# Optimization experiments

Measured on AMD Instinct MI355X. Metric: run time of the kernel, lower is better.

Reference implementation:

```python
import jax, jax.numpy as jnp
import numpy as np

B, Hc, Wc, C, NH, SR, WS = 4, 64, 64, 256, 8, 2, 4
N = Hc * Wc


def _window_partition(x, ws, H, W):
    # x: (B, h, N, d) -> (B*h*nWin, ws*ws, d)
    Bb, h, _, d = x.shape
    x = x.reshape(Bb * h, H // ws, ws, W // ws, ws, d)
    x = x.transpose(0, 1, 3, 2, 4, 5)
    return x.reshape(-1, ws * ws, d)


def _window_reverse(win, ws, H, W, head):
    nwin = (H // ws) * (W // ws)
    Bh = win.shape[0] // nwin
    x = win.reshape(Bh, H // ws, W // ws, ws, ws, -1).transpose(0, 1, 3, 2, 4, 5).reshape(Bh, H, W, -1)
    Bb = Bh // head
    x = x.reshape(Bb, head, H, W, -1).transpose(0, 2, 3, 1, 4)  # heads interleave into channels
    return x.reshape(Bb, H * W, -1)


def _layernorm(x, w, b):
    m = x.mean(-1, keepdims=True)
    v = x.var(-1, keepdims=True)
    return (x - m) / jnp.sqrt(v + 1e-5) * w + b


def setup_inputs() -> dict:
    key = jax.random.key(0)
    ks = jax.random.split(key, 16)
    lin = lambda k, i, o: 0.02 * jax.random.normal(k, (i, o), jnp.float32)
    inp = {
        'x': jax.random.normal(ks[0], (B, N, C), jnp.float32),
        'q1_w': lin(ks[1], C, C // 2), 'q1_b': jnp.zeros((C // 2,), jnp.float32),
        'kv1_w': lin(ks[2], C, C), 'kv1_b': jnp.zeros((C,), jnp.float32),
        'q2_w': lin(ks[3], C, C // 2), 'q2_b': jnp.zeros((C // 2,), jnp.float32),
        'kv2_w': lin(ks[4], C, C), 'kv2_b': jnp.zeros((C,), jnp.float32),
        'lepe_w': lin(ks[5], C, C), 'lepe_b': jnp.zeros((C,), jnp.float32),
        'lepe_conv_w': jnp.sqrt(2.0 / 9.0) * jax.random.normal(ks[6], (C, 1, 3, 3), jnp.float32),
        'lepe_conv_b': jnp.zeros((C,), jnp.float32),
        'sr_w': jnp.sqrt(2.0 / (SR * SR * C)) * jax.random.normal(ks[7], (C, C, SR, SR), jnp.float32),
        'sr_b': jnp.zeros((C,), jnp.float32),
        'norm_w': jnp.ones((C,), jnp.float32), 'norm_b': jnp.zeros((C,), jnp.float32),
        'proj_w': lin(ks[8], C, C), 'proj_b': jnp.zeros((C,), jnp.float32),
        'H': Hc, 'W': Wc,
    }
    return inp


def reference(x, q1_w, q1_b, kv1_w, kv1_b, q2_w, q2_b, kv2_w, kv2_b,
              lepe_w, lepe_b, lepe_conv_w, lepe_conv_b, sr_w, sr_b,
              norm_w, norm_b, proj_w, proj_b, H, W):
    Bb, Nn, Cc = x.shape
    h2 = NH // 2
    d = Cc // NH
    sr = sr_w.shape[-1]
    scale = d ** -0.5
    ws = WS

    # lepe: linear -> depthwise 3x3 conv
    l = (x @ lepe_w + lepe_b).transpose(0, 2, 1).reshape(Bb, Cc, H, W)
    l = jax.lax.conv_general_dilated(l, lepe_conv_w, (1, 1), ((1, 1), (1, 1)),
                                     dimension_numbers=('NCHW', 'OIHW', 'NCHW'),
                                     feature_group_count=Cc) + lepe_conv_b[None, :, None, None]
    lepe = l.reshape(Bb, Cc, Nn).transpose(0, 2, 1)

    # branch 1: spatial-reduction global attention
    q1 = (x @ q1_w + q1_b).reshape(Bb, Nn, h2, d).transpose(0, 2, 1, 3)
    x_img = x.transpose(0, 2, 1).reshape(Bb, Cc, H, W)
    xs = jax.lax.conv_general_dilated(x_img, sr_w, (sr, sr), 'VALID',
                                      dimension_numbers=('NCHW', 'OIHW', 'NCHW')) + sr_b[None, :, None, None]
    N1 = (H // sr) * (W // sr)
    xs = xs.reshape(Bb, Cc, N1).transpose(0, 2, 1)
    xs = jax.nn.gelu(_layernorm(xs, norm_w, norm_b), approximate=False)
    kv1 = (xs @ kv1_w + kv1_b).reshape(Bb, N1, 2, h2, d).transpose(2, 0, 3, 1, 4)
    k1, v1 = kv1[0], kv1[1]
    attn1 = jax.nn.softmax(jnp.einsum('bhnd,bhmd->bhnm', q1, k1) * scale, axis=-1)
    x1 = jnp.einsum('bhnm,bhmd->bnhd', attn1, v1).reshape(Bb, Nn, Cc // 2)
    g = jax.lax.stop_gradient(attn1).mean(1).mean(1).reshape(Bb, H // sr, W // sr)
    g = jnp.repeat(jnp.repeat(g, sr, axis=1), sr, axis=2)  # nearest upsample to (B,H,W)

    # branch 2: Swin-style windowed attention (window 4)
    q2 = (x @ q2_w + q2_b).reshape(Bb, Nn, h2, d).transpose(0, 2, 1, 3)
    kv2 = (x @ kv2_w + kv2_b).reshape(Bb, Nn, 2, h2, d).transpose(2, 0, 3, 1, 4)
    k2, v2 = kv2[0], kv2[1]
    q2w = _window_partition(q2, ws, H, W)
    k2w = _window_partition(k2, ws, H, W)
    v2w = _window_partition(v2, ws, H, W)
    attn2 = jax.nn.softmax(jnp.einsum('wnd,wmd->wnm', q2w, k2w) * scale, axis=-1)
    x2 = jnp.einsum('wnm,wmd->wnd', attn2, v2w)
    x2 = _window_reverse(x2, ws, H, W, h2)
    nwin = (H // ws) * (W // ws)
    lm = jax.lax.stop_gradient(attn2).reshape(Bb, h2, nwin, ws * ws, ws * ws).mean(1).mean(2)
    lm = lm.reshape(Bb, H // ws, W // ws, ws, ws).transpose(0, 1, 3, 2, 4).reshape(Bb, H, W)

    out = jnp.concatenate([x1, x2], axis=-1)
    p = (out + lepe) @ proj_w + proj_b
    out = p + p  # proj_drop is identity at p=0.0, so x = drop(p) + p = 2p

    mask = lm + g
    mask1 = mask.reshape(Bb, H * W)
    mask2 = mask.transpose(0, 2, 1).reshape(Bb, H * W)
    return out, mask1, mask2
```

## Files before the change

### kernel.cpp

```cpp
#include <hip/hip_runtime.h>
#include <hip/hip_bf16.h>
#include <math.h>

typedef __hip_bfloat16 bf16;
typedef __attribute__((ext_vector_type(8))) short bf16x8;
typedef __attribute__((ext_vector_type(4))) short bf16x4;
typedef __attribute__((ext_vector_type(4))) float f32x4;

__device__ __forceinline__ float b2f(bf16 v) { return __bfloat162float(v); }
__device__ __forceinline__ bf16  f2b(float v) { return __float2bfloat16(v); }
__device__ __forceinline__ float s2f(short v) { return __uint_as_float(((unsigned)(unsigned short)v) << 16); }

__device__ __forceinline__ void gl_lds16(const void* g, void* l)
{
    __builtin_amdgcn_global_load_lds(
        (const __attribute__((address_space(1))) void*)g,
        (__attribute__((address_space(3))) void*)l, 16, 0, 0);
}

__global__ void detect_dtype(const void* x, int* flag)
{
    __shared__ int cnt;
    if (threadIdx.x == 0) cnt = 0;
    __syncthreads();
    const unsigned* w = (const unsigned*)x;
    int sane = 0;
    for (int i = threadIdx.x; i < 2048; i += 256) {
        unsigned lo = (w[i] & 0xFFFFu) << 16;
        float v = __uint_as_float(lo);
        float a = fabsf(v);
        if (v == 0.f || (a > 1e-8f && a < 1e4f)) sane++;
    }
    atomicAdd(&cnt, sane);
    __syncthreads();
    if (threadIdx.x == 0) *flag = (cnt < 1640) ? 1 : 0;
}

struct AllArgs {
    const void* x; bf16* cx;
    const void* srw;  bf16* srwT;
    const void* dww;  bf16* dwT;
    const void* psrc[10]; bf16* pdst[10]; int pn[10];
    const void* wsrc[6]; bf16* wdst[6]; int wN[6]; int wblkoff[7];
    float* gbuf;
};
__global__ void convert_all(AllArgs a, const int* __restrict__ flag)
{
    int blk = blockIdx.x, t = threadIdx.x;
    int fl = *flag;
    if (blk < 4096) {
        int i = blk * 256 + t;
        if (fl) {
            float4 v = ((const float4*)a.x)[i];
            bf16 tmp[4];
            tmp[0] = f2b(v.x); tmp[1] = f2b(v.y); tmp[2] = f2b(v.z); tmp[3] = f2b(v.w);
            *(bf16x4*)&a.cx[i * 4] = *(bf16x4*)tmp;
        } else {
            ((bf16x4*)a.cx)[i] = ((const bf16x4*)a.x)[i];
        }
    } else if (blk < 5120) {
        int o = (blk - 4096) * 256 + t;
        int co = o >> 10, kg = o & 1023;
        int e = kg >> 8, ci = kg & 255;
        int si = co * 1024 + ci * 4 + e;
        float v = fl ? ((const float*)a.srw)[si] : s2f(((const short*)a.srw)[si]);
        a.srwT[o] = f2b(v);
    } else if (blk < 5129) {
        int o = (blk - 5120) * 256 + t;
        if (o >= 2304) return;
        int k = o >> 8, c = o & 255;
        float v = fl ? ((const float*)a.dww)[c * 9 + k] : s2f(((const short*)a.dww)[c * 9 + k]);
        a.dwT[o] = f2b(v);
    } else if (blk < 5139) {
        int bi = blk - 5129;
        int n = a.pn[bi];
        const void* s = a.psrc[bi];
        bf16* d = a.pdst[bi];
        for (int i = t; i < n; i += 256)
            d[i] = fl ? f2b(((const float*)s)[i]) : f2b(s2f(((const short*)s)[i]));
    } else if (blk < 6419) {
        int wblk = blk - 5139;
        int ti = 0;
        while (wblk >= a.wblkoff[ti + 1]) ++ti;
        int o = (wblk - a.wblkoff[ti]) * 256 + t;
        int n = o >> 8, k = o & 255;
        int N = a.wN[ti];
        float v = fl ? ((const float*)a.wsrc[ti])[k * N + n]
                     : s2f(((const short*)a.wsrc[ti])[k * N + n]);
        a.wdst[ti][o] = f2b(v);
    } else {
        for (int i = t; i < 4096; i += 256) a.gbuf[i] = 0.f;
    }
}

__device__ __forceinline__ void qkv_body(
    int bx, int by, char* smem,
    const bf16* __restrict__ A, const bf16* __restrict__ WT, const bf16* __restrict__ bias,
    bf16* __restrict__ Cl, bf16* __restrict__ Cq1, bf16* __restrict__ Cq2, bf16* __restrict__ Ckv2)
{
    char* As = smem;
    char* Bs = smem + 8192;
    int t = threadIdx.x;
    int m0 = bx * 128, ybase = by * 128;
    int w = t >> 6, l = t & 63, lane16 = l & 15, quad = l >> 4;
    int wr = w >> 1, wc = w & 1;

    int oph0 = w * 2048 + l * 16;
    int oph1 = oph0 + 1024;
    int olog0 = oph0 ^ (((oph0 >> 7) & 3) << 4);
    int olog1 = oph1 ^ (((oph1 >> 7) & 3) << 4);
    int row0 = olog0 >> 6, ce0 = (olog0 & 63) >> 1;
    int row1 = olog1 >> 6, ce1 = (olog1 & 63) >> 1;
    char* asb0 = As + w * 2048; char* asb1 = asb0 + 1024;
    char* bsb0 = Bs + w * 2048; char* bsb1 = bsb0 + 1024;

    f32x4 acc[4][4] = {};
    for (int k0 = 0; k0 < 256; k0 += 32) {
        gl_lds16(&A[(size_t)(m0 + row0) * 256 + k0 + ce0], asb0);
        gl_lds16(&A[(size_t)(m0 + row1) * 256 + k0 + ce1], asb1);
        gl_lds16(&WT[(size_t)(ybase + row0) * 256 + k0 + ce0], bsb0);
        gl_lds16(&WT[(size_t)(ybase + row1) * 256 + k0 + ce1], bsb1);
        __syncthreads();
        bf16x8 a[4], b[4];
        #pragma unroll
        for (int i = 0; i < 4; ++i) {
            int ra = wr * 64 + i * 16 + lane16;
            int oa = (ra << 6) + (quad << 4);
            oa ^= (((oa >> 7) & 3) << 4);
            a[i] = *(const bf16x8*)(As + oa);
            int rb = wc * 64 + i * 16 + lane16;
            int ob = (rb << 6) + (quad << 4);
            ob ^= (((ob >> 7) & 3) << 4);
            b[i] = *(const bf16x8*)(Bs + ob);
        }
        #pragma unroll
        for (int i = 0; i < 4; ++i)
            #pragma unroll
            for (int j = 0; j < 4; ++j)
                acc[i][j] = __builtin_amdgcn_mfma_f32_16x16x32_bf16(a[i], b[j], acc[i][j], 0, 0, 0);
        __syncthreads();
    }
    bf16* C; int N, cbase;
    if (ybase < 256)      { C = Cl;   N = 256; cbase = ybase; }
    else if (ybase < 384) { C = Cq1;  N = 128; cbase = ybase - 256; }
    else if (ybase < 512) { C = Cq2;  N = 128; cbase = ybase - 384; }
    else                  { C = Ckv2; N = 256; cbase = ybase - 512; }
    float mult = (ybase >= 256 && ybase < 512)
               ? (0.17677669529663687f * 1.4426950408889634f) : 1.f;
    #pragma unroll
    for (int j = 0; j < 4; ++j) {
        int gcol = ybase + wc * 64 + j * 16 + lane16;
        float bv = b2f(bias[gcol]);
        int col = cbase + wc * 64 + j * 16 + lane16;
        #pragma unroll
        for (int i = 0; i < 4; ++i)
            #pragma unroll
            for (int r = 0; r < 4; ++r) {
                int row = m0 + wr * 64 + i * 16 + quad * 4 + r;
                C[(size_t)row * N + col] = f2b((acc[i][j][r] + bv) * mult);
            }
    }
}

__device__ __forceinline__ void sr_body(
    int bx, int by, char* smem,
    const bf16* __restrict__ x, const bf16* __restrict__ WT,
    const bf16* __restrict__ bias, bf16* __restrict__ C)
{
    bf16 (*As)[40] = (bf16(*)[40])smem;
    bf16 (*Bs)[40] = (bf16(*)[40])(smem + 5120);
    int t = threadIdx.x;
    int m0 = bx * 64, n0 = by * 64;
    int w = t >> 6, l = t & 63, lane16 = l & 15, quad = l >> 4;
    int sr = t >> 2, sc = (t & 3) * 8;
    int brow = m0 + sr;
    int b = brow >> 10, p = brow & 1023;
    int pi = p >> 5, pj = p & 31;
    f32x4 acc[4] = {};
    for (int k0 = 0; k0 < 1024; k0 += 32) {
        int kg = k0 + sc;
        int e = kg >> 8, ci = kg & 255;
        int di = e >> 1, dj = e & 1;
        int n = (2 * pi + di) * 64 + 2 * pj + dj;
        *(bf16x8*)&As[sr][sc] = *(const bf16x8*)&x[(size_t)((b << 12) + n) * 256 + ci];
        *(bf16x8*)&Bs[sr][sc] = *(const bf16x8*)&WT[(size_t)(n0 + sr) * 1024 + kg];
        __syncthreads();
        bf16x8 a = *(const bf16x8*)&As[w * 16 + lane16][quad * 8];
        #pragma unroll
        for (int ct = 0; ct < 4; ++ct) {
            bf16x8 bb = *(const bf16x8*)&Bs[ct * 16 + lane16][quad * 8];
            acc[ct] = __builtin_amdgcn_mfma_f32_16x16x32_bf16(a, bb, acc[ct], 0, 0, 0);
        }
        __syncthreads();
    }
    #pragma unroll
    for (int ct = 0; ct < 4; ++ct) {
        int col = n0 + ct * 16 + lane16;
        float bv = b2f(bias[col]);
        #pragma unroll
        for (int r = 0; r < 4; ++r) {
            int row = m0 + w * 16 + quad * 4 + r;
            C[(size_t)row * 256 + col] = f2b(acc[ct][r] + bv);
        }
    }
}

__global__ __launch_bounds__(256) void fuseA(
    const bf16* __restrict__ cx, const bf16* __restrict__ wTqkv, const bf16* __restrict__ bcat,
    bf16* __restrict__ Cl, bf16* __restrict__ Cq1, bf16* __restrict__ Cq2, bf16* __restrict__ Ckv2,
    const bf16* __restrict__ srwT, const bf16* __restrict__ srb, bf16* __restrict__ xs_pre)
{
    __shared__ __align__(16) char smem[16384];
    int idx = blockIdx.x;
    int g = idx >> 2, r3 = idx & 3;
    if (r3 < 3) {
        int q = g * 3 + r3;
        qkv_body(q & 127, q >> 7, smem, cx, wTqkv, bcat, Cl, Cq1, Cq2, Ckv2);
    } else {
        sr_body(g & 63, g >> 6, smem, cx, srwT, srb, xs_pre);
    }
}

__device__ __forceinline__ void ln_body(
    int blk,
    const bf16* __restrict__ xin, const bf16* __restrict__ nw,
    const bf16* __restrict__ nb, bf16* __restrict__ xout)
{
    int w = threadIdx.x >> 6, lane = threadIdx.x & 63;
    int r = blk * 4 + w;
    bf16x4 xv = *(const bf16x4*)&xin[(size_t)r * 256 + lane * 4];
    float v[4];
    #pragma unroll
    for (int j = 0; j < 4; ++j) v[j] = s2f(xv[j]);
    float s = v[0] + v[1] + v[2] + v[3];
    #pragma unroll
    for (int o = 1; o <= 32; o <<= 1) s += __shfl_xor(s, o);
    float mean = s * (1.f / 256.f);
    float ss = 0.f;
    #pragma unroll
    for (int j = 0; j < 4; ++j) { float d = v[j] - mean; ss += d * d; }
    #pragma unroll
    for (int o = 1; o <= 32; o <<= 1) ss += __shfl_xor(ss, o);
    float inv = rsqrtf(ss * (1.f / 256.f) + 1e-5f);
    bf16x4 wv = *(const bf16x4*)&nw[lane * 4];
    bf16x4 bv = *(const bf16x4*)&nb[lane * 4];
    bf16 ov[4];
    #pragma unroll
    for (int j = 0; j < 4; ++j) {
        float y = (v[j] - mean) * inv * s2f(wv[j]) + s2f(bv[j]);
        ov[j] = f2b(0.5f * y * (1.f + erff(y * 0.70710678118654752f)));
    }
    *(bf16x4*)&xout[(size_t)r * 256 + lane * 4] = *(bf16x4*)ov;
}

__device__ __forceinline__ void dw_body(
    int blk,
    const bf16* __restrict__ lin, const bf16* __restrict__ dwT,
    const bf16* __restrict__ bias, bf16* __restrict__ out)
{
    int tid = blk * 256 + threadIdx.x;
    int c0 = (tid & 31) * 8;
    int j  = (tid >> 5) & 63;
    int i  = ((tid >> 11) & 31) * 2;
    int b  = tid >> 16;
    float acc0[8], acc1[8];
    bf16x8 bv = *(const bf16x8*)&bias[c0];
    #pragma unroll
    for (int q = 0; q < 8; ++q) { acc0[q] = s2f(bv[q]); acc1[q] = s2f(bv[q]); }
    bf16x8 wv[3][3];
    #pragma unroll
    for (int di = 0; di < 3; ++di)
        #pragma unroll
        for (int dj = 0; dj < 3; ++dj)
            wv[di][dj] = *(const bf16x8*)&dwT[(di * 3 + dj) * 256 + c0];
    #pragma unroll
    for (int r = -1; r <= 2; ++r) {
        int ii = i + r;
        if (ii < 0 || ii > 63) continue;
        #pragma unroll
        for (int dj = 0; dj < 3; ++dj) {
            int jj = j + dj - 1;
            if (jj < 0 || jj > 63) continue;
            bf16x8 xv = *(const bf16x8*)&lin[(size_t)((b << 12) + ii * 64 + jj) * 256 + c0];
            if (r <= 1) {
                bf16x8 w0 = wv[r + 1][dj];
                #pragma unroll
                for (int q = 0; q < 8; ++q) acc0[q] += s2f(xv[q]) * s2f(w0[q]);
            }
            if (r >= 0) {
                bf16x8 w1 = wv[r][dj];
                #pragma unroll
                for (int q = 0; q < 8; ++q) acc1[q] += s2f(xv[q]) * s2f(w1[q]);
            }
        }
    }
    bf16 ov[8];
    #pragma unroll
    for (int q = 0; q < 8; ++q) ov[q] = f2b(acc0[q]);
    *(bf16x8*)&out[(size_t)((b << 12) + i * 64 + j) * 256 + c0] = *(bf16x8*)ov;
    #pragma unroll
    for (int q = 0; q < 8; ++q) ov[q] = f2b(acc1[q]);
    *(bf16x8*)&out[(size_t)((b << 12) + (i + 1) * 64 + j) * 256 + c0] = *(bf16x8*)ov;
}

__global__ __launch_bounds__(256) void fuseB(
    const bf16* __restrict__ xs_pre, const bf16* __restrict__ nw,
    const bf16* __restrict__ nb, bf16* __restrict__ xs,
    const bf16* __restrict__ lepe_lin, const bf16* __restrict__ dwT,
    const bf16* __restrict__ dwb, bf16* __restrict__ lepe)
{
    int idx = blockIdx.x;
    if ((idx & 1) == 0) ln_body(idx >> 1, xs_pre, nw, nb, xs);
    else                dw_body(idx >> 1, lepe_lin, dwT, dwb, lepe);
}

__global__ __launch_bounds__(256) void gemm_kv1(
    const bf16* __restrict__ A, const bf16* __restrict__ WT, const bf16* __restrict__ bias,
    bf16* __restrict__ k1, bf16* __restrict__ v1T)
{
    __shared__ bf16 As[64][40];
    __shared__ bf16 Bs[64][40];
    int t = threadIdx.x;
    int m0 = blockIdx.x * 64, n0 = blockIdx.y * 64;
    int w = t >> 6, l = t & 63, lane16 = l & 15, quad = l >> 4;
    int sr = t >> 2, sc = (t & 3) * 8;
    f32x4 acc[4] = {};
    for (int k0 = 0; k0 < 256; k0 += 32) {
        *(bf16x8*)&As[sr][sc] = *(const bf16x8*)&A[(size_t)(m0 + sr) * 256 + k0 + sc];
        *(bf16x8*)&Bs[sr][sc] = *(const bf16x8*)&WT[(size_t)(n0 + sr) * 256 + k0 + sc];
        __syncthreads();
        bf16x8 a = *(const bf16x8*)&As[w * 16 + lane16][quad * 8];
        #pragma unroll
        for (int ct = 0; ct < 4; ++ct) {
            bf16x8 b = *(const bf16x8*)&Bs[ct * 16 + lane16][quad * 8];
            acc[ct] = __builtin_amdgcn_mfma_f32_16x16x32_bf16(a, b, acc[ct], 0, 0, 0);
        }
        __syncthreads();
    }
    #pragma unroll
    for (int ct = 0; ct < 4; ++ct) {
        int col = n0 + ct * 16 + lane16;
        float bv = b2f(bias[col]);
        #pragma unroll
        for (int r = 0; r < 4; ++r) {
            int row = m0 + w * 16 + quad * 4 + r;
            float val = acc[ct][r] + bv;
            int bb = row >> 10, key = row & 1023;
            if (col < 128) {
                k1[(size_t)row * 128 + col] = f2b(val);
            } else {
                int h = (col - 128) >> 5, ch = (col - 128) & 31;
                v1T[(size_t)((bb * 4 + h) * 32 + ch) * 1024 + key] = f2b(val);
            }
        }
    }
}

__global__ __launch_bounds__(256) void attn1_split(
    const bf16* __restrict__ q1, const bf16* __restrict__ k1,
    const bf16* __restrict__ v1T, bf16* __restrict__ attn_out, float* __restrict__ g)
{
    __shared__ bf16 Kt[2][64][40];
    __shared__ bf16 Vt[2][32][68];
    __shared__ bf16 PTT[4][16][68];
    __shared__ float gp[1024];

    int t = threadIdx.x;
    int blk = blockIdx.x;
    int qc = blk & 63, h = (blk >> 6) & 3, b = blk >> 8;
    int n0 = qc * 64;
    int w = t >> 6, l = t & 63, lane16 = l & 15, quad = l >> 4;

    const bf16* Kbase = k1 + (size_t)b * 1024 * 128 + 32 * h;
    const bf16* Vbase = v1T + (size_t)((b * 4 + h) * 32) * 1024;
    bf16x8 qa = *(const bf16x8*)&q1[(size_t)(b * 4096 + n0 + 16 * w + lane16) * 128 + 32 * h + quad * 8];

    for (int i = t; i < 1024; i += 256) gp[i] = 0.f;

    int sr = t >> 2, sc = (t & 3) * 8;
    int vrow = t >> 3, vcol = (t & 7) * 8;
    bf16* ptt = &PTT[w][0][0];

    *(bf16x8*)&Kt[0][sr][sc]     = *(const bf16x8*)&Kbase[(size_t)sr * 128 + sc];
    *(bf16x8*)&Vt[0][vrow][vcol] = *(const bf16x8*)&Vbase[(size_t)vrow * 1024 + vcol];
    __syncthreads();

    float lacc = 0.f;
    f32x4 oT0 = {}, oT1 = {};

    for (int ktl = 0; ktl < 16; ++ktl) {
        int cur = ktl & 1;
        bf16x8 knext, vnext;
        if (ktl < 15) {
            knext = *(const bf16x8*)&Kbase[(size_t)((ktl + 1) * 64 + sr) * 128 + sc];
            vnext = *(const bf16x8*)&Vbase[(size_t)vrow * 1024 + (ktl + 1) * 64 + vcol];
        }
        bf16x8 kf[4];
        #pragma unroll
        for (int st = 0; st < 4; ++st)
            kf[st] = *(const bf16x8*)&Kt[cur][st * 16 + lane16][quad * 8];
        #pragma unroll
        for (int st = 0; st < 4; ++st) {
            f32x4 z = {0.f, 0.f, 0.f, 0.f};
            f32x4 sT = __builtin_amdgcn_mfma_f32_16x16x32_bf16(kf[st], qa, z, 0, 0, 0);
            bf16 pk[4];
            #pragma unroll
            for (int r = 0; r < 4; ++r) {
                float p = exp2f(sT[r]);
                lacc += p;
                pk[r] = f2b(p);
            }
            *(bf16x4*)&ptt[lane16 * 68 + st * 16 + quad * 4] = *(bf16x4*)pk;
        }
        #pragma unroll
        for (int kh = 0; kh < 2; ++kh) {
            bf16x8 pf  = *(const bf16x8*)&ptt[lane16 * 68 + kh * 32 + quad * 8];
            bf16x8 vf0 = *(const bf16x8*)&Vt[cur][lane16][kh * 32 + quad * 8];
            bf16x8 vf1 = *(const bf16x8*)&Vt[cur][16 + lane16][kh * 32 + quad * 8];
            oT0 = __builtin_amdgcn_mfma_f32_16x16x32_bf16(vf0, pf, oT0, 0, 0, 0);
            oT1 = __builtin_amdgcn_mfma_f32_16x16x32_bf16(vf1, pf, oT1, 0, 0, 0);
        }
        if (ktl < 15) {
            *(bf16x8*)&Kt[cur ^ 1][sr][sc]     = knext;
            *(bf16x8*)&Vt[cur ^ 1][vrow][vcol] = vnext;
        }
        __syncthreads();
    }

    lacc += __shfl_xor(lacc, 16);
    lacc += __shfl_xor(lacc, 32);
    float rl = 1.f / lacc;
    {
        bf16 ov0[4], ov1[4];
        #pragma unroll
        for (int r = 0; r < 4; ++r) {
            ov0[r] = f2b(oT0[r] * rl);
            ov1[r] = f2b(oT1[r] * rl);
        }
        size_t ro = (size_t)(b * 4096 + n0 + 16 * w + lane16) * 256 + 32 * h;
        *(bf16x4*)&attn_out[ro + quad * 4]      = *(bf16x4*)ov0;
        *(bf16x4*)&attn_out[ro + 16 + quad * 4] = *(bf16x4*)ov1;
    }

    float rlq[4];
    #pragma unroll
    for (int r = 0; r < 4; ++r) rlq[r] = __shfl(rl, quad * 4 + r);

    *(bf16x8*)&Kt[0][sr][sc] = *(const bf16x8*)&Kbase[(size_t)sr * 128 + sc];
    __syncthreads();
    for (int ktl = 0; ktl < 16; ++ktl) {
        int cur = ktl & 1;
        bf16x8 knext;
        if (ktl < 15)
            knext = *(const bf16x8*)&Kbase[(size_t)((ktl + 1) * 64 + sr) * 128 + sc];
        bf16x8 kf2[4];
        #pragma unroll
        for (int st = 0; st < 4; ++st)
            kf2[st] = *(const bf16x8*)&Kt[cur][st * 16 + lane16][quad * 8];
        #pragma unroll
        for (int st = 0; st < 4; ++st) {
            f32x4 z = {0.f, 0.f, 0.f, 0.f};
            f32x4 s = __builtin_amdgcn_mfma_f32_16x16x32_bf16(qa, kf2[st], z, 0, 0, 0);
            float cs = 0.f;
            #pragma unroll
            for (int r = 0; r < 4; ++r) cs += exp2f(s[r]) * rlq[r];
            cs += __shfl_xor(cs, 16);
            cs += __shfl_xor(cs, 32);
            if (quad == 0) atomicAdd(&gp[ktl * 64 + st * 16 + lane16], cs);
        }
        if (ktl < 15)
            *(bf16x8*)&Kt[cur ^ 1][sr][sc] = knext;
        __syncthreads();
    }

    for (int i = t; i < 1024; i += 256)
        atomicAdd(&g[(b << 10) + i], gp[i] * (1.f / 16384.f));
}

__global__ __launch_bounds__(256) void attn2_mfma(
    const bf16* __restrict__ q2, const bf16* __restrict__ kv2,
    bf16* __restrict__ attn_out, float* __restrict__ lm)
{
    __shared__ bf16 PT2[4][16 * 40];
    __shared__ float lmw[16];
    int t = threadIdx.x;
    int blk = blockIdx.x;
    int b = blk >> 8, win = blk & 255;
    int wi = win >> 4, wj = win & 15;
    int h = t >> 6, l = t & 63, lane16 = l & 15, quad = l >> 4;

    if (t < 16) lmw[t] = 0.f;
    bf16* ptt = &PT2[h][0];
    {
        bf16 zz[4] = {};
        *(bf16x4*)&ptt[lane16 * 40 + 16 + quad * 4] = *(bf16x4*)zz;
    }
    __syncthreads();

    size_t base = (size_t)(b * 4096);
    int r0 = wi * 4, c0w = wj * 4;
    int tq = (r0 + (lane16 >> 2)) * 64 + c0w + (lane16 & 3);

    bf16x8 qa = *(const bf16x8*)&q2[(base + tq) * 128 + h * 32 + quad * 8];
    bf16x8 kf = *(const bf16x8*)&kv2[(base + tq) * 256 + h * 32 + quad * 8];

    f32x4 z = {0.f, 0.f, 0.f, 0.f};
    f32x4 sT = __builtin_amdgcn_mfma_f32_16x16x32_bf16(kf, qa, z, 0, 0, 0);
    float sv[4];
    #pragma unroll
    for (int r = 0; r < 4; ++r) sv[r] = sT[r];
    float mx = fmaxf(fmaxf(sv[0], sv[1]), fmaxf(sv[2], sv[3]));
    mx = fmaxf(mx, __shfl_xor(mx, 16));
    mx = fmaxf(mx, __shfl_xor(mx, 32));
    float p[4], lsum = 0.f;
    #pragma unroll
    for (int r = 0; r < 4; ++r) { p[r] = exp2f(sv[r] - mx); lsum += p[r]; }
    lsum += __shfl_xor(lsum, 16);
    lsum += __shfl_xor(lsum, 32);
    float rl = 1.f / lsum;
    bf16 pk[4];
    #pragma unroll
    for (int r = 0; r < 4; ++r) { p[r] *= rl; pk[r] = f2b(p[r]); }
    *(bf16x4*)&ptt[lane16 * 40 + quad * 4] = *(bf16x4*)pk;

    bf16x8 vf0 = {}, vf1 = {};
    if (quad < 2) {
        #pragma unroll
        for (int jj = 0; jj < 8; ++jj) {
            int key = quad * 8 + jj;
            int tk = (r0 + (key >> 2)) * 64 + c0w + (key & 3);
            const short* vp = (const short*)&kv2[(base + tk) * 256 + 128 + h * 32];
            vf0[jj] = vp[lane16];
            vf1[jj] = vp[16 + lane16];
        }
    }
    bf16x8 pf = *(const bf16x8*)&ptt[lane16 * 40 + quad * 8];
    f32x4 o0 = __builtin_amdgcn_mfma_f32_16x16x32_bf16(vf0, pf, z, 0, 0, 0);
    f32x4 o1 = __builtin_amdgcn_mfma_f32_16x16x32_bf16(vf1, pf, z, 0, 0, 0);
    {
        bf16 ov0[4], ov1[4];
        #pragma unroll
        for (int r = 0; r < 4; ++r) { ov0[r] = f2b(o0[r]); ov1[r] = f2b(o1[r]); }
        bf16* op = attn_out + (base + tq) * 256 + 128 + h * 32;
        *(bf16x4*)&op[quad * 4]      = *(bf16x4*)ov0;
        *(bf16x4*)&op[16 + quad * 4] = *(bf16x4*)ov1;
    }

    #pragma unroll
    for (int r = 0; r < 4; ++r) {
        float c = p[r];
        c += __shfl_xor(c, 1);
        c += __shfl_xor(c, 2);
        c += __shfl_xor(c, 4);
        c += __shfl_xor(c, 8);
        if (lane16 == 0) atomicAdd(&lmw[quad * 4 + r], c);
    }
    __syncthreads();
    if (t < 16) {
        int nk = (r0 + (t >> 2)) * 64 + c0w + (t & 3);
        lm[(b << 12) + nk] = lmw[t] * (1.f / 64.f);
    }
}

__global__ __launch_bounds__(256) void gemm_proj128(
    const bf16* __restrict__ A, const bf16* __restrict__ A2,
    const bf16* __restrict__ WT, const bf16* __restrict__ bias,
    const float* __restrict__ lm, const float* __restrict__ g,
    void* __restrict__ dout, const int* __restrict__ flag)
{
    if (blockIdx.y == 2) {
        if (blockIdx.x >= 64) return;
        int tid = blockIdx.x * 256 + threadIdx.x;
        int b = tid >> 12, n = tid & 4095;
        int i = n >> 6, j = n & 63;
        float v = lm[tid] + g[(b << 10) + (i >> 1) * 32 + (j >> 1)];
        size_t o1 = (size_t)4194304 + (b << 12) + i * 64 + j;
        size_t o2 = (size_t)4194304 + 16384 + (b << 12) + j * 64 + i;
        if (*flag) { ((float*)dout)[o1] = v; ((float*)dout)[o2] = v; }
        else       { ((bf16*)dout)[o1] = f2b(v); ((bf16*)dout)[o2] = f2b(v); }
        return;
    }
    __shared__ bf16 As[128][40];
    __shared__ bf16 Bs[128][40];
    int t = threadIdx.x;
    int m0 = blockIdx.x * 128, n0 = blockIdx.y * 128;
    int w = t >> 6, l = t & 63, lane16 = l & 15, quad = l >> 4;
    int wr = w >> 1, wc = w & 1;
    int sr = t >> 1, sc = (t & 1) * 16;
    f32x4 acc[4][4] = {};
    for (int k0 = 0; k0 < 256; k0 += 32) {
        #pragma unroll
        for (int hh = 0; hh < 2; ++hh) {
            bf16x8 va = *(const bf16x8*)&A[(size_t)(m0 + sr) * 256 + k0 + sc + hh * 8];
            bf16x8 vb = *(const bf16x8*)&A2[(size_t)(m0 + sr) * 256 + k0 + sc + hh * 8];
            bf16 tmp[8];
            #pragma unroll
            for (int q = 0; q < 8; ++q) tmp[q] = f2b(s2f(va[q]) + s2f(vb[q]));
            *(bf16x8*)&As[sr][sc + hh * 8] = *(bf16x8*)tmp;
        }
        *(bf16x8*)&Bs[sr][sc]     = *(const bf16x8*)&WT[(size_t)(n0 + sr) * 256 + k0 + sc];
        *(bf16x8*)&Bs[sr][sc + 8] = *(const bf16x8*)&WT[(size_t)(n0 + sr) * 256 + k0 + sc + 8];
        __syncthreads();
        bf16x8 a[4], b[4];
        #pragma unroll
        for (int i = 0; i < 4; ++i) {
            a[i] = *(const bf16x8*)&As[wr * 64 + i * 16 + lane16][quad * 8];
            b[i] = *(const bf16x8*)&Bs[wc * 64 + i * 16 + lane16][quad * 8];
        }
        #pragma unroll
        for (int i = 0; i < 4; ++i)
            #pragma unroll
            for (int j = 0; j < 4; ++j)
                acc[i][j] = __builtin_amdgcn_mfma_f32_16x16x32_bf16(a[i], b[j], acc[i][j], 0, 0, 0);
        __syncthreads();
    }
    #pragma unroll
    for (int j = 0; j < 4; ++j) {
        int col = n0 + wc * 64 + j * 16 + lane16;
        float bv = b2f(bias[col]);
        #pragma unroll
        for (int i = 0; i < 4; ++i)
            #pragma unroll
            for (int r = 0; r < 4; ++r) {
                int row = m0 + wr * 64 + i * 16 + quad * 4 + r;
                float rv = (acc[i][j][r] + bv) * 2.f;
                size_t o = (size_t)row * 256 + col;
                if (*flag) ((float*)dout)[o] = rv;
                else       ((bf16*)dout)[o] = f2b(rv);
            }
    }
}

extern "C" void kernel_launch(void* const* d_in, const int* in_sizes, int n_in,
                              void* d_out, int out_size, void* d_ws, size_t ws_size,
                              hipStream_t stream)
{
    char* ws = (char*)d_ws;
    size_t off = 0;
    auto alloc = [&](size_t bytes) {
        void* p = ws + off;
        off += (bytes + 255) & ~(size_t)255;
        return p;
    };
    bf16* cx       = (bf16*)alloc((size_t)4194304 * 2);
    bf16* lepe_lin = (bf16*)alloc((size_t)4194304 * 2);
    bf16* attn_out = lepe_lin;
    bf16* lepe     = (bf16*)alloc((size_t)4194304 * 2);
    bf16* q1buf    = (bf16*)alloc((size_t)2097152 * 2);
    bf16* q2buf    = (bf16*)alloc((size_t)2097152 * 2);
    bf16* kv2buf   = (bf16*)alloc((size_t)4194304 * 2);
    bf16* xs_pre   = (bf16*)alloc((size_t)1048576 * 2);
    bf16* k1buf    = xs_pre;
    bf16* v1Tbuf   = xs_pre + 524288;
    bf16* xs       = (bf16*)alloc((size_t)1048576 * 2);
    bf16* wTqkv    = (bf16*)alloc((size_t)196608 * 2);
    bf16* kv1_wT   = (bf16*)alloc(65536 * 2);
    bf16* proj_wT  = (bf16*)alloc(65536 * 2);
    bf16* sr_wT    = (bf16*)alloc(262144 * 2);
    bf16* dwT      = (bf16*)alloc(2304 * 2);
    bf16* bcat     = (bf16*)alloc(768 * 2);
    bf16* ckv1b    = (bf16*)alloc(256 * 2);
    bf16* csrb     = (bf16*)alloc(256 * 2);
    bf16* cnw      = (bf16*)alloc(256 * 2);
    bf16* cnb      = (bf16*)alloc(256 * 2);
    bf16* cpb      = (bf16*)alloc(256 * 2);
    bf16* clcb     = (bf16*)alloc(256 * 2);
    float* gbuf    = (float*)alloc(4096 * 4);
    float* lmbuf   = (float*)alloc(16384 * 4);
    int*   flag    = (int*)alloc(256);

    detect_dtype<<<1, 256, 0, stream>>>(d_in[0], flag);

    AllArgs aa;
    aa.x = d_in[0]; aa.cx = cx;
    aa.srw = d_in[13]; aa.srwT = sr_wT;
    aa.dww = d_in[11]; aa.dwT = dwT;
    aa.psrc[0] = d_in[10]; aa.pdst[0] = bcat;       aa.pn[0] = 256;
    aa.psrc[1] = d_in[2];  aa.pdst[1] = bcat + 256; aa.pn[1] = 128;
    aa.psrc[2] = d_in[6];  aa.pdst[2] = bcat + 384; aa.pn[2] = 128;
    aa.psrc[3] = d_in[8];  aa.pdst[3] = bcat + 512; aa.pn[3] = 256;
    aa.psrc[4] = d_in[4];  aa.pdst[4] = ckv1b;      aa.pn[4] = 256;
    aa.psrc[5] = d_in[14]; aa.pdst[5] = csrb;       aa.pn[5] = 256;
    aa.psrc[6] = d_in[15]; aa.pdst[6] = cnw;        aa.pn[6] = 256;
    aa.psrc[7] = d_in[16]; aa.pdst[7] = cnb;        aa.pn[7] = 256;
    aa.psrc[8] = d_in[18]; aa.pdst[8] = cpb;        aa.pn[8] = 256;
    aa.psrc[9] = d_in[12]; aa.pdst[9] = clcb;       aa.pn[9] = 256;
    aa.wsrc[0] = d_in[9];  aa.wdst[0] = wTqkv;             aa.wN[0] = 256;
    aa.wsrc[1] = d_in[1];  aa.wdst[1] = wTqkv + 256 * 256; aa.wN[1] = 128;
    aa.wsrc[2] = d_in[5];  aa.wdst[2] = wTqkv + 384 * 256; aa.wN[2] = 128;
    aa.wsrc[3] = d_in[7];  aa.wdst[3] = wTqkv + 512 * 256; aa.wN[3] = 256;
    aa.wsrc[4] = d_in[3];  aa.wdst[4] = kv1_wT;            aa.wN[4] = 256;
    aa.wsrc[5] = d_in[17]; aa.wdst[5] = proj_wT;           aa.wN[5] = 256;
    int bo[7] = {0, 256, 384, 512, 768, 1024, 1280};
    for (int i = 0; i < 7; ++i) aa.wblkoff[i] = bo[i];
    aa.gbuf = gbuf;
    convert_all<<<6420, 256, 0, stream>>>(aa, flag);

    fuseA<<<1024, 256, 0, stream>>>(cx, wTqkv, bcat, lepe_lin, q1buf, q2buf, kv2buf,
                                    sr_wT, csrb, xs_pre);
    fuseB<<<2048, 256, 0, stream>>>(xs_pre, cnw, cnb, xs, lepe_lin, dwT, clcb, lepe);
    gemm_kv1<<<dim3(64, 4), 256, 0, stream>>>(xs, kv1_wT, ckv1b, k1buf, v1Tbuf);
    attn1_split<<<1024, 256, 0, stream>>>(q1buf, k1buf, v1Tbuf, attn_out, gbuf);
    attn2_mfma<<<1024, 256, 0, stream>>>(q2buf, kv2buf, attn_out, lmbuf);
    gemm_proj128<<<dim3(128, 3), 256, 0, stream>>>(attn_out, lepe, proj_wT, cpb,
                                                   lmbuf, gbuf, d_out, flag);
}
```

Baseline: 259.1 us.

## Fuse input fp32-to-bf16 conversion into QKV and SR GEMM loads; use native exp2

Removes the separate conversion pass that turned the x tensor into a bf16 copy. The QKV and spatial-reduction GEMMs now read x directly and convert fp32 to bf16 while staging into LDS. The A tile moves from async global_load_lds with a swizzle to register loads into a padded LDS array. This saves a 16 MB read/write round trip, but the GEMMs now read twice the bytes and lose the async LDS load path. exp2f calls are also replaced with the amdgcn exp2 builtin.

```diff
diff --git a/kernel.cpp b/kernel.cpp
--- a/kernel.cpp
+++ b/kernel.cpp
@@ -10,6 +10,7 @@
 __device__ __forceinline__ float b2f(bf16 v) { return __bfloat162float(v); }
 __device__ __forceinline__ bf16  f2b(float v) { return __float2bfloat16(v); }
 __device__ __forceinline__ float s2f(short v) { return __uint_as_float(((unsigned)(unsigned short)v) << 16); }
+__device__ __forceinline__ float ex2(float x) { return __builtin_amdgcn_exp2f(x); }
 
 __device__ __forceinline__ void gl_lds16(const void* g, void* l)
 {
@@ -37,7 +38,6 @@
 }
 
 struct AllArgs {
-    const void* x; bf16* cx;
     const void* srw;  bf16* srwT;
     const void* dww;  bf16* dwT;
     const void* psrc[10]; bf16* pdst[10]; int pn[10];
@@ -48,38 +48,28 @@
 {
     int blk = blockIdx.x, t = threadIdx.x;
     int fl = *flag;
-    if (blk < 4096) {
-        int i = blk * 256 + t;
-        if (fl) {
-            float4 v = ((const float4*)a.x)[i];
-            bf16 tmp[4];
-            tmp[0] = f2b(v.x); tmp[1] = f2b(v.y); tmp[2] = f2b(v.z); tmp[3] = f2b(v.w);
-            *(bf16x4*)&a.cx[i * 4] = *(bf16x4*)tmp;
-        } else {
-            ((bf16x4*)a.cx)[i] = ((const bf16x4*)a.x)[i];
-        }
-    } else if (blk < 5120) {
-        int o = (blk - 4096) * 256 + t;
+    if (blk < 1024) {
+        int o = blk * 256 + t;
         int co = o >> 10, kg = o & 1023;
         int e = kg >> 8, ci = kg & 255;
         int si = co * 1024 + ci * 4 + e;
         float v = fl ? ((const float*)a.srw)[si] : s2f(((const short*)a.srw)[si]);
         a.srwT[o] = f2b(v);
-    } else if (blk < 5129) {
-        int o = (blk - 5120) * 256 + t;
+    } else if (blk < 1033) {
+        int o = (blk - 1024) * 256 + t;
         if (o >= 2304) return;
         int k = o >> 8, c = o & 255;
         float v = fl ? ((const float*)a.dww)[c * 9 + k] : s2f(((const short*)a.dww)[c * 9 + k]);
         a.dwT[o] = f2b(v);
-    } else if (blk < 5139) {
-        int bi = blk - 5129;
+    } else if (blk < 1043) {
+        int bi = blk - 1033;
         int n = a.pn[bi];
         const void* s = a.psrc[bi];
         bf16* d = a.pdst[bi];
         for (int i = t; i < n; i += 256)
             d[i] = fl ? f2b(((const float*)s)[i]) : f2b(s2f(((const short*)s)[i]));
-    } else if (blk < 6419) {
-        int wblk = blk - 5139;
+    } else if (blk < 2323) {
+        int wblk = blk - 1043;
         int ti = 0;
         while (wblk >= a.wblkoff[ti + 1]) ++ti;
         int o = (wblk - a.wblkoff[ti]) * 256 + t;
@@ -94,16 +84,17 @@
 }
 
 __device__ __forceinline__ void qkv_body(
-    int bx, int by, char* smem,
-    const bf16* __restrict__ A, const bf16* __restrict__ WT, const bf16* __restrict__ bias,
+    int bx, int by, char* smem, int fl,
+    const void* __restrict__ x, const bf16* __restrict__ WT, const bf16* __restrict__ bias,
     bf16* __restrict__ Cl, bf16* __restrict__ Cq1, bf16* __restrict__ Cq2, bf16* __restrict__ Ckv2)
 {
-    char* As = smem;
-    char* Bs = smem + 8192;
+    bf16 (*As)[40] = (bf16(*)[40])smem;
+    char* Bs = smem + 10240;
     int t = threadIdx.x;
     int m0 = bx * 128, ybase = by * 128;
     int w = t >> 6, l = t & 63, lane16 = l & 15, quad = l >> 4;
     int wr = w >> 1, wc = w & 1;
+    int srow = t >> 1, scol = (t & 1) * 16;
 
     int oph0 = w * 2048 + l * 16;
     int oph1 = oph0 + 1024;
@@ -111,23 +102,34 @@
     int olog1 = oph1 ^ (((oph1 >> 7) & 3) << 4);
     int row0 = olog0 >> 6, ce0 = (olog0 & 63) >> 1;
     int row1 = olog1 >> 6, ce1 = (olog1 & 63) >> 1;
-    char* asb0 = As + w * 2048; char* asb1 = asb0 + 1024;
     char* bsb0 = Bs + w * 2048; char* bsb1 = bsb0 + 1024;
+
+    const float* xf = (const float*)x;
+    const bf16*  xb = (const bf16*)x;
 
     f32x4 acc[4][4] = {};
     for (int k0 = 0; k0 < 256; k0 += 32) {
-        gl_lds16(&A[(size_t)(m0 + row0) * 256 + k0 + ce0], asb0);
-        gl_lds16(&A[(size_t)(m0 + row1) * 256 + k0 + ce1], asb1);
+        if (fl) {
+            const float4* p = (const float4*)&xf[(size_t)(m0 + srow) * 256 + k0 + scol];
+            float4 v0 = p[0], v1 = p[1], v2 = p[2], v3 = p[3];
+            bf16 tmp[16];
+            tmp[0]=f2b(v0.x); tmp[1]=f2b(v0.y); tmp[2]=f2b(v0.z); tmp[3]=f2b(v0.w);
+            tmp[4]=f2b(v1.x); tmp[5]=f2b(v1.y); tmp[6]=f2b(v1.z); tmp[7]=f2b(v1.w);
+            tmp[8]=f2b(v2.x); tmp[9]=f2b(v2.y); tmp[10]=f2b(v2.z); tmp[11]=f2b(v2.w);
+            tmp[12]=f2b(v3.x); tmp[13]=f2b(v3.y); tmp[14]=f2b(v3.z); tmp[15]=f2b(v3.w);
+            *(bf16x8*)&As[srow][scol]     = *(bf16x8*)&tmp[0];
+            *(bf16x8*)&As[srow][scol + 8] = *(bf16x8*)&tmp[8];
+        } else {
+            *(bf16x8*)&As[srow][scol]     = *(const bf16x8*)&xb[(size_t)(m0 + srow) * 256 + k0 + scol];
+            *(bf16x8*)&As[srow][scol + 8] = *(const bf16x8*)&xb[(size_t)(m0 + srow) * 256 + k0 + scol + 8];
+        }
         gl_lds16(&WT[(size_t)(ybase + row0) * 256 + k0 + ce0], bsb0);
         gl_lds16(&WT[(size_t)(ybase + row1) * 256 + k0 + ce1], bsb1);
         __syncthreads();
         bf16x8 a[4], b[4];
         #pragma unroll
         for (int i = 0; i < 4; ++i) {
-            int ra = wr * 64 + i * 16 + lane16;
-            int oa = (ra << 6) + (quad << 4);
-            oa ^= (((oa >> 7) & 3) << 4);
-            a[i] = *(const bf16x8*)(As + oa);
+            a[i] = *(const bf16x8*)&As[wr * 64 + i * 16 + lane16][quad * 8];
             int rb = wc * 64 + i * 16 + lane16;
             int ob = (rb << 6) + (quad << 4);
             ob ^= (((ob >> 7) & 3) << 4);
@@ -163,8 +165,8 @@
 }
 
 __device__ __forceinline__ void sr_body(
-    int bx, int by, char* smem,
-    const bf16* __restrict__ x, const bf16* __restrict__ WT,
+    int bx, int by, char* smem, int fl,
+    const void* __restrict__ x, const bf16* __restrict__ WT,
     const bf16* __restrict__ bias, bf16* __restrict__ C)
 {
     bf16 (*As)[40] = (bf16(*)[40])smem;
@@ -176,13 +178,25 @@
     int brow = m0 + sr;
     int b = brow >> 10, p = brow & 1023;
     int pi = p >> 5, pj = p & 31;
+    const float* xf = (const float*)x;
+    const bf16*  xb = (const bf16*)x;
     f32x4 acc[4] = {};
     for (int k0 = 0; k0 < 1024; k0 += 32) {
         int kg = k0 + sc;
         int e = kg >> 8, ci = kg & 255;
         int di = e >> 1, dj = e & 1;
         int n = (2 * pi + di) * 64 + 2 * pj + dj;
-        *(bf16x8*)&As[sr][sc] = *(const bf16x8*)&x[(size_t)((b << 12) + n) * 256 + ci];
+        size_t off = (size_t)((b << 12) + n) * 256 + ci;
+        if (fl) {
+            const float4* pp = (const float4*)&xf[off];
+            float4 v0 = pp[0], v1 = pp[1];
+            bf16 tmp[8];
+            tmp[0]=f2b(v0.x); tmp[1]=f2b(v0.y); tmp[2]=f2b(v0.z); tmp[3]=f2b(v0.w);
+            tmp[4]=f2b(v1.x); tmp[5]=f2b(v1.y); tmp[6]=f2b(v1.z); tmp[7]=f2b(v1.w);
+            *(bf16x8*)&As[sr][sc] = *(bf16x8*)tmp;
+        } else {
+            *(bf16x8*)&As[sr][sc] = *(const bf16x8*)&xb[off];
+        }
         *(bf16x8*)&Bs[sr][sc] = *(const bf16x8*)&WT[(size_t)(n0 + sr) * 1024 + kg];
         __syncthreads();
         bf16x8 a = *(const bf16x8*)&As[w * 16 + lane16][quad * 8];
@@ -206,18 +220,20 @@
 }
 
 __global__ __launch_bounds__(256) void fuseA(
-    const bf16* __restrict__ cx, const bf16* __restrict__ wTqkv, const bf16* __restrict__ bcat,
+    const void* __restrict__ x, const int* __restrict__ flag,
+    const bf16* __restrict__ wTqkv, const bf16* __restrict__ bcat,
     bf16* __restrict__ Cl, bf16* __restrict__ Cq1, bf16* __restrict__ Cq2, bf16* __restrict__ Ckv2,
     const bf16* __restrict__ srwT, const bf16* __restrict__ srb, bf16* __restrict__ xs_pre)
 {
-    __shared__ __align__(16) char smem[16384];
+    __shared__ __align__(16) char smem[18432];
+    int fl = *flag;
     int idx = blockIdx.x;
     int g = idx >> 2, r3 = idx & 3;
     if (r3 < 3) {
         int q = g * 3 + r3;
-        qkv_body(q & 127, q >> 7, smem, cx, wTqkv, bcat, Cl, Cq1, Cq2, Ckv2);
+        qkv_body(q & 127, q >> 7, smem, fl, x, wTqkv, bcat, Cl, Cq1, Cq2, Ckv2);
     } else {
-        sr_body(g & 63, g >> 6, smem, cx, srwT, srb, xs_pre);
+        sr_body(g & 63, g >> 6, smem, fl, x, srwT, srb, xs_pre);
     }
 }
 
@@ -406,7 +422,7 @@
             bf16 pk[4];
             #pragma unroll
             for (int r = 0; r < 4; ++r) {
-                float p = exp2f(sT[r]);
+                float p = ex2(sT[r]);
                 lacc += p;
                 pk[r] = f2b(p);
             }
@@ -463,7 +479,7 @@
             f32x4 s = __builtin_amdgcn_mfma_f32_16x16x32_bf16(qa, kf2[st], z, 0, 0, 0);
             float cs = 0.f;
             #pragma unroll
-            for (int r = 0; r < 4; ++r) cs += exp2f(s[r]) * rlq[r];
+            for (int r = 0; r < 4; ++r) cs += ex2(s[r]) * rlq[r];
             cs += __shfl_xor(cs, 16);
             cs += __shfl_xor(cs, 32);
             if (quad == 0) atomicAdd(&gp[ktl * 64 + st * 16 + lane16], cs);
@@ -514,7 +530,7 @@
     mx = fmaxf(mx, __shfl_xor(mx, 32));
     float p[4], lsum = 0.f;
     #pragma unroll
-    for (int r = 0; r < 4; ++r) { p[r] = exp2f(sv[r] - mx); lsum += p[r]; }
+    for (int r = 0; r < 4; ++r) { p[r] = ex2(sv[r] - mx); lsum += p[r]; }
     lsum += __shfl_xor(lsum, 16);
     lsum += __shfl_xor(lsum, 32);
     float rl = 1.f / lsum;
@@ -642,7 +658,6 @@
         off += (bytes + 255) & ~(size_t)255;
         return p;
     };
-    bf16* cx       = (bf16*)alloc((size_t)4194304 * 2);
     bf16* lepe_lin = (bf16*)alloc((size_t)4194304 * 2);
     bf16* attn_out = lepe_lin;
     bf16* lepe     = (bf16*)alloc((size_t)4194304 * 2);
@@ -672,7 +687,6 @@
     detect_dtype<<<1, 256, 0, stream>>>(d_in[0], flag);
 
     AllArgs aa;
-    aa.x = d_in[0]; aa.cx = cx;
     aa.srw = d_in[13]; aa.srwT = sr_wT;
     aa.dww = d_in[11]; aa.dwT = dwT;
     aa.psrc[0] = d_in[10]; aa.pdst[0] = bcat;       aa.pn[0] = 256;
@@ -694,9 +708,10 @@
     int bo[7] = {0, 256, 384, 512, 768, 1024, 1280};
     for (int i = 0; i < 7; ++i) aa.wblkoff[i] = bo[i];
     aa.gbuf = gbuf;
-    convert_all<<<6420, 256, 0, stream>>>(aa, flag);
-
-    fuseA<<<1024, 256, 0, stream>>>(cx, wTqkv, bcat, lepe_lin, q1buf, q2buf, kv2buf,
+    convert_all<<<2324, 256, 0, stream>>>(aa, flag);
+
+    fuseA<<<1024, 256, 0, stream>>>(d_in[0], flag, wTqkv, bcat,
+                                    lepe_lin, q1buf, q2buf, kv2buf,
                                     sr_wT, csrb, xs_pre);
     fuseB<<<2048, 256, 0, stream>>>(xs_pre, cnw, cnb, xs, lepe_lin, dwT, clcb, lepe);
     gemm_kv1<<<dim3(64, 4), 256, 0, stream>>>(xs, kv1_wT, ckv1b, k1buf, v1Tbuf);
```

Result: slower. 273.4 us (+5.5%).
